# Optimization experiments

Measured on AMD Instinct MI355X. Metric: run time of the kernel, lower is better.

## Reference

```python
import jax, jax.numpy as jnp
import numpy as np

B, C, H, W = 4, 64, 64, 64  # in_dim hardcoded to 64 by the module's views


def _conv1x1(x, w, b):
    # x: [B,C,H,W], w: [O,C], b: [O]
    return jnp.einsum('bchw,oc->bohw', x, w) + b[None, :, None, None]


def _branch(x, wq, bq, wk, bk, wv, bv):
    b_, c_, h_, w_ = x.shape
    n = h_ * w_
    q = _conv1x1(x, wq, bq).reshape(b_, c_, n)
    k = _conv1x1(x, wk, bk).reshape(b_, c_, n)
    v = _conv1x1(x, wv, bv).reshape(b_, c_, n)
    # scores[b,i,j] = sum_c q[b,c,i] * k[b,c,j]  (no scale factor, as in source)
    s = jax.nn.softmax(jnp.einsum('bci,bcj->bij', q, k), axis=-1)  # [B,N,N]
    # out[b,c,j] = sum_i v[b,c,i] * s[b,i,j]
    return jnp.einsum('bci,bij->bcj', v, s).reshape(b_, c_, h_, w_)


def setup_inputs() -> dict:
    key = jax.random.key(0)
    ks = jax.random.split(key, 17)
    sc = 1.0 / np.sqrt(C)
    d = {'x': jax.random.normal(ks[0], (B, C, H, W), jnp.float32)}
    names = ['qh', 'kh', 'vh', 'ql', 'kl', 'vl']
    for i, nm in enumerate(names):
        d['W_' + nm] = jax.random.normal(ks[1 + 2 * i], (C, C), jnp.float32) * sc
        d['b_' + nm] = jax.random.normal(ks[2 + 2 * i], (C,), jnp.float32) * 0.01
    d['g1'] = jax.random.normal(ks[13], (1,), jnp.float32) * 0.5
    d['g2'] = jax.random.normal(ks[14], (1,), jnp.float32) * 0.5
    d['W_f'] = jax.random.normal(ks[15], (C, 2 * C), jnp.float32) * (1.0 / np.sqrt(2 * C))
    d['b_f'] = jax.random.normal(ks[16], (C,), jnp.float32) * 0.01
    return d


def reference(x, W_qh, b_qh, W_kh, b_kh, W_vh, b_vh, W_ql, b_ql, W_kl, b_kl, W_vl, b_vl, g1, g2, W_f, b_f):
    xh1 = g1[0] * _branch(x, W_qh, b_qh, W_kh, b_kh, W_vh, b_vh)
    xl1 = g2[0] * _branch(x, W_ql, b_ql, W_kl, b_kl, W_vl, b_vl)
    cat = jnp.concatenate([xh1, xl1], axis=1)  # [B,2C,H,W]
    return _conv1x1(cat, W_f, b_f)
```

## Files before the change

### kernel.cpp

```cpp
#include <hip/hip_runtime.h>

#define NN 4096
#define CD 64

typedef __attribute__((ext_vector_type(8))) short bf16x8;
typedef __attribute__((ext_vector_type(4))) float f32x4;

__device__ unsigned short g_Qh[2][4][NN][CD];
__device__ unsigned short g_Ql[2][4][NN][CD];
__device__ unsigned short g_Kh[2][4][NN][CD];
__device__ unsigned short g_Kl[2][4][NN][CD];
__device__ float          g_Vf[2][4][CD][NN];
__device__ unsigned short g_Vh[2][4][CD][NN];
__device__ unsigned short g_Vl[2][4][CD][NN];
__device__ float          g_O [2][4][CD][NN];
__device__ float          g_Z [2][4][NN];

__device__ inline f32x4 mfma16(bf16x8 a, bf16x8 b, f32x4 c) {
  return __builtin_amdgcn_mfma_f32_16x16x32_bf16(a, b, c, 0, 0, 0);
}

__device__ inline void split_bf(float x, unsigned short& h, unsigned short& l) {
  unsigned u = __builtin_bit_cast(unsigned, x);
  h = (unsigned short)(u >> 16);
  float hf = __builtin_bit_cast(float, u & 0xffff0000u);
  unsigned v = __builtin_bit_cast(unsigned, x - hf);
  v += 0x7fffu + ((v >> 16) & 1u);
  l = (unsigned short)(v >> 16);
}

__device__ inline void lds_barrier() {
  asm volatile("s_waitcnt lgkmcnt(0)\n\ts_barrier" ::: "memory");
}

struct ProjArgs {
  const float* x;
  const float* W[6];
  const float* bias[6];
};

__global__ __launch_bounds__(256) void proj_kernel(ProjArgs a) {
  __shared__ float Wt[64][68];
  __shared__ float bs[64];
  const int tid = threadIdx.x;
  const int m = blockIdx.z;
  const float* __restrict__ W = a.W[m];
#pragma unroll
  for (int k = 0; k < 16; ++k) {
    int t = k * 256 + tid;
    Wt[t & 63][t >> 6] = W[t];
  }
  if (tid < 64) bs[tid] = a.bias[m][tid];
  __syncthreads();

  const int b = blockIdx.y;
  const int n = (blockIdx.x << 6) + (tid & 63);
  const int og = tid >> 6;
  const float* __restrict__ xp = a.x + ((size_t)b * CD) * NN + n;

  float acc[16];
#pragma unroll
  for (int k = 0; k < 16; ++k) acc[k] = bs[og * 16 + k];

#pragma unroll 4
  for (int c = 0; c < 64; ++c) {
    float xv = xp[(size_t)c * NN];
    float w[16];
    *(float4*)&w[0]  = *(const float4*)&Wt[c][og * 16 + 0];
    *(float4*)&w[4]  = *(const float4*)&Wt[c][og * 16 + 4];
    *(float4*)&w[8]  = *(const float4*)&Wt[c][og * 16 + 8];
    *(float4*)&w[12] = *(const float4*)&Wt[c][og * 16 + 12];
#pragma unroll
    for (int k = 0; k < 16; ++k) acc[k] += w[k] * xv;
  }

  const int br = m / 3, kind = m % 3;
  if (kind == 2) {
    float* dst = &g_Vf[br][b][0][0] + n;
#pragma unroll
    for (int k = 0; k < 16; ++k) dst[(size_t)(og * 16 + k) * NN] = acc[k];
  } else {
    unsigned short hi[16], lo[16];
#pragma unroll
    for (int k = 0; k < 16; ++k) split_bf(acc[k], hi[k], lo[k]);
    unsigned short* dh = (kind == 0) ? &g_Qh[br][b][n][og * 16] : &g_Kh[br][b][n][og * 16];
    unsigned short* dl = (kind == 0) ? &g_Ql[br][b][n][og * 16] : &g_Kl[br][b][n][og * 16];
    *(uint4*)dh       = *(const uint4*)&hi[0];
    *(uint4*)(dh + 8) = *(const uint4*)&hi[8];
    *(uint4*)dl       = *(const uint4*)&lo[0];
    *(uint4*)(dl + 8) = *(const uint4*)&lo[8];
  }
}

__global__ __launch_bounds__(256) void pass1_kernel() {
  __shared__ unsigned short ks_h[2][64 * 64];
  __shared__ unsigned short ks_l[2][64 * 64];
  __shared__ float zbuf[2][64];

  const int tid = threadIdx.x;
  const int bid = blockIdx.x;
  const int img = bid & 7;
  const int br = img >> 2, b = img & 3;
  const int i0 = (bid >> 3) << 6;

  const int lane = tid & 63, w = tid >> 6;
  const int wi = w >> 1, wj = w & 1;
  const int lm = lane & 15, q = lane >> 4;

  const unsigned short* __restrict__ QhB = &g_Qh[br][b][0][0];
  const unsigned short* __restrict__ QlB = &g_Ql[br][b][0][0];
  const unsigned short* __restrict__ KhB = &g_Kh[br][b][0][0];
  const unsigned short* __restrict__ KlB = &g_Kl[br][b][0][0];

  bf16x8 qa[2][2][2];
#pragma unroll
  for (int it = 0; it < 2; ++it)
#pragma unroll
    for (int cs = 0; cs < 2; ++cs) {
      size_t off = (size_t)(i0 + wi * 32 + it * 16 + lm) * 64 + cs * 32 + q * 8;
      qa[it][cs][0] = *(const bf16x8*)(QhB + off);
      qa[it][cs][1] = *(const bf16x8*)(QlB + off);
    }

  const int r0 = tid >> 3, s0 = tid & 7;
  const int r1 = (256 + tid) >> 3, s1 = tid & 7;
  const int la0 = r0 * 128 + ((s0 * 16) ^ ((r0 & 7) << 4));
  const int la1 = r1 * 128 + ((s1 * 16) ^ ((r1 & 7) << 4));
  const size_t g0 = (size_t)r0 * 64 + s0 * 8;
  const size_t g1o = (size_t)r1 * 64 + s1 * 8;

  uint4 ph0, ph1, pl0, pl1;
  ph0 = *(const uint4*)(KhB + g0); ph1 = *(const uint4*)(KhB + g1o);
  pl0 = *(const uint4*)(KlB + g0); pl1 = *(const uint4*)(KlB + g1o);
  *(uint4*)((char*)ks_h[0] + la0) = ph0; *(uint4*)((char*)ks_h[0] + la1) = ph1;
  *(uint4*)((char*)ks_l[0] + la0) = pl0; *(uint4*)((char*)ks_l[0] + la1) = pl1;
  ph0 = *(const uint4*)(KhB + 4096 + g0); ph1 = *(const uint4*)(KhB + 4096 + g1o);
  pl0 = *(const uint4*)(KlB + 4096 + g0); pl1 = *(const uint4*)(KlB + 4096 + g1o);
  lds_barrier();

  float zacc[2][4];
#pragma unroll
  for (int it = 0; it < 2; ++it)
#pragma unroll
    for (int r = 0; r < 4; ++r) zacc[it][r] = 0.f;

  for (int t = 0; t < 64; ++t) {
    const int cur = t & 1;
    if (t < 63) {
      *(uint4*)((char*)ks_h[cur ^ 1] + la0) = ph0;
      *(uint4*)((char*)ks_h[cur ^ 1] + la1) = ph1;
      *(uint4*)((char*)ks_l[cur ^ 1] + la0) = pl0;
      *(uint4*)((char*)ks_l[cur ^ 1] + la1) = pl1;
      if (t < 62) {
        size_t tb = (size_t)(t + 2) * 4096;
        ph0 = *(const uint4*)(KhB + tb + g0); ph1 = *(const uint4*)(KhB + tb + g1o);
        pl0 = *(const uint4*)(KlB + tb + g0); pl1 = *(const uint4*)(KlB + tb + g1o);
      }
    }

    bf16x8 kb[2][2][2];
#pragma unroll
    for (int jt = 0; jt < 2; ++jt) {
      int row = wj * 32 + jt * 16 + lm;
      int rb = row * 128, sw = (row & 7) << 4;
#pragma unroll
      for (int cs = 0; cs < 2; ++cs) {
        int byte = rb + ((cs * 64 + q * 16) ^ sw);
        kb[jt][cs][0] = *(const bf16x8*)((const char*)ks_h[cur] + byte);
        kb[jt][cs][1] = *(const bf16x8*)((const char*)ks_l[cur] + byte);
      }
    }

    const f32x4 zf = {0.f, 0.f, 0.f, 0.f};
#pragma unroll
    for (int it = 0; it < 2; ++it)
#pragma unroll
      for (int jt = 0; jt < 2; ++jt) {
        f32x4 s = mfma16(qa[it][0][0], kb[jt][0][0], zf);
        s = mfma16(qa[it][1][0], kb[jt][1][0], s);
        s = mfma16(qa[it][0][0], kb[jt][0][1], s);
        s = mfma16(qa[it][1][0], kb[jt][1][1], s);
        s = mfma16(qa[it][0][1], kb[jt][0][0], s);
        s = mfma16(qa[it][1][1], kb[jt][1][0], s);
        zacc[it][0] += __expf(s[0]);
        zacc[it][1] += __expf(s[1]);
        zacc[it][2] += __expf(s[2]);
        zacc[it][3] += __expf(s[3]);
      }
    lds_barrier();
  }

#pragma unroll
  for (int mm = 1; mm < 16; mm <<= 1)
#pragma unroll
    for (int it = 0; it < 2; ++it)
#pragma unroll
      for (int r = 0; r < 4; ++r) zacc[it][r] += __shfl_xor(zacc[it][r], mm, 64);

  if (lm == 0) {
#pragma unroll
    for (int it = 0; it < 2; ++it)
#pragma unroll
      for (int r = 0; r < 4; ++r)
        zbuf[wj][wi * 32 + it * 16 + q * 4 + r] = zacc[it][r];
  }
  __syncthreads();
  if (tid < 64) g_Z[br][b][i0 + tid] = zbuf[0][tid] + zbuf[1][tid];
}

__global__ __launch_bounds__(256) void scalev_kernel(const float* __restrict__ g1,
                                                     const float* __restrict__ g2) {
  int idx = blockIdx.x * 256 + threadIdx.x;
  int i4 = idx & 1023;
  int c  = (idx >> 10) & 63;
  int b  = (idx >> 16) & 3;
  int br = idx >> 18;
  float g = br ? g2[0] : g1[0];
  const float4 z = *(const float4*)&g_Z[br][b][i4 * 4];
  float4 v = *(const float4*)&g_Vf[br][b][c][i4 * 4];
  float vv[4] = {v.x * g / z.x, v.y * g / z.y, v.z * g / z.z, v.w * g / z.w};
  unsigned short h[4], l[4];
#pragma unroll
  for (int r = 0; r < 4; ++r) split_bf(vv[r], h[r], l[r]);
  uint2 uh, ul;
  uh.x = (unsigned)h[0] | ((unsigned)h[1] << 16);
  uh.y = (unsigned)h[2] | ((unsigned)h[3] << 16);
  ul.x = (unsigned)l[0] | ((unsigned)l[1] << 16);
  ul.y = (unsigned)l[2] | ((unsigned)l[3] << 16);
  *(uint2*)&g_Vh[br][b][c][i4 * 4] = uh;
  *(uint2*)&g_Vl[br][b][c][i4 * 4] = ul;
}

__global__ __launch_bounds__(256, 2) void pass2_kernel() {
  __shared__ unsigned short pt_h[64 * 64];
  __shared__ unsigned short pt_l[64 * 64];

  const int tid = threadIdx.x;
  const int bid = blockIdx.x;
  const int img = bid & 7;
  const int br = img >> 2, b = img & 3;
  const int j0 = (bid >> 3) << 6;

  const int lane = tid & 63, w = tid >> 6;
  const int wi = w >> 1, wj = w & 1;
  const int lm = lane & 15, q = lane >> 4;

  const unsigned short* __restrict__ QhB = &g_Qh[br][b][0][0];
  const unsigned short* __restrict__ QlB = &g_Ql[br][b][0][0];
  const unsigned short* __restrict__ KhB = &g_Kh[br][b][0][0];
  const unsigned short* __restrict__ KlB = &g_Kl[br][b][0][0];
  const unsigned short* __restrict__ VhB = &g_Vh[br][b][0][0];
  const unsigned short* __restrict__ VlB = &g_Vl[br][b][0][0];

  bf16x8 kb[2][2][2];
#pragma unroll
  for (int jt = 0; jt < 2; ++jt)
#pragma unroll
    for (int cs = 0; cs < 2; ++cs) {
      size_t off = (size_t)(j0 + wj * 32 + jt * 16 + lm) * 64 + cs * 32 + q * 8;
      kb[jt][cs][0] = *(const bf16x8*)(KhB + off);
      kb[jt][cs][1] = *(const bf16x8*)(KlB + off);
    }

  bf16x8 qa[2][2][2];
  bf16x8 va[2][2][2];
  auto loadQ = [&](int ib) {
#pragma unroll
    for (int it = 0; it < 2; ++it)
#pragma unroll
      for (int cs = 0; cs < 2; ++cs) {
        size_t off = (size_t)(ib + wi * 32 + it * 16 + lm) * 64 + cs * 32 + q * 8;
        qa[it][cs][0] = *(const bf16x8*)(QhB + off);
        qa[it][cs][1] = *(const bf16x8*)(QlB + off);
      }
  };
  auto loadV = [&](int ib) {
#pragma unroll
    for (int ct = 0; ct < 2; ++ct)
#pragma unroll
      for (int ks = 0; ks < 2; ++ks) {
        size_t off = (size_t)(wi * 32 + ct * 16 + lm) * NN + ib + ks * 32 + q * 8;
        va[ct][ks][0] = *(const bf16x8*)(VhB + off);
        va[ct][ks][1] = *(const bf16x8*)(VlB + off);
      }
  };
  loadQ(0);
  loadV(0);

  f32x4 oacc[2][2];
#pragma unroll
  for (int ct = 0; ct < 2; ++ct)
#pragma unroll
    for (int jt = 0; jt < 2; ++jt) oacc[ct][jt] = (f32x4){0.f, 0.f, 0.f, 0.f};

  for (int t = 0; t < 64; ++t) {
    const int i0 = t << 6;
    const f32x4 zf = {0.f, 0.f, 0.f, 0.f};
    f32x4 sacc[2][2];
#pragma unroll
    for (int it = 0; it < 2; ++it)
#pragma unroll
      for (int jt = 0; jt < 2; ++jt) {
        f32x4 s = mfma16(qa[it][0][0], kb[jt][0][0], zf);
        s = mfma16(qa[it][1][0], kb[jt][1][0], s);
        s = mfma16(qa[it][0][0], kb[jt][0][1], s);
        s = mfma16(qa[it][1][0], kb[jt][1][1], s);
        s = mfma16(qa[it][0][1], kb[jt][0][0], s);
        s = mfma16(qa[it][1][1], kb[jt][1][0], s);
        sacc[it][jt] = s;
      }
    if (t < 63) loadQ(i0 + 64);

    uint2 wh[2][2], wl[2][2];
#pragma unroll
    for (int it = 0; it < 2; ++it)
#pragma unroll
      for (int jt = 0; jt < 2; ++jt) {
        unsigned short h[4], l[4];
#pragma unroll
        for (int r = 0; r < 4; ++r) {
          float e = __expf(sacc[it][jt][r]);
          split_bf(e, h[r], l[r]);
        }
        wh[it][jt].x = (unsigned)h[0] | ((unsigned)h[1] << 16);
        wh[it][jt].y = (unsigned)h[2] | ((unsigned)h[3] << 16);
        wl[it][jt].x = (unsigned)l[0] | ((unsigned)l[1] << 16);
        wl[it][jt].y = (unsigned)l[2] | ((unsigned)l[3] << 16);
      }

    lds_barrier();
#pragma unroll
    for (int it = 0; it < 2; ++it)
#pragma unroll
      for (int jt = 0; jt < 2; ++jt) {
        int row = wj * 32 + jt * 16 + lm;
        int byte = row * 128 + (((wi * 64) + it * 32 + q * 8) ^ ((row & 7) << 4));
        *(uint2*)((char*)pt_h + byte) = wh[it][jt];
        *(uint2*)((char*)pt_l + byte) = wl[it][jt];
      }
    lds_barrier();

    bf16x8 pb[2][2][2];
#pragma unroll
    for (int jt = 0; jt < 2; ++jt) {
      int row = wj * 32 + jt * 16 + lm;
      int rb = row * 128, sw = (row & 7) << 4;
#pragma unroll
      for (int ks = 0; ks < 2; ++ks) {
        int byte = rb + ((ks * 64 + q * 16) ^ sw);
        pb[jt][ks][0] = *(const bf16x8*)((const char*)pt_h + byte);
        pb[jt][ks][1] = *(const bf16x8*)((const char*)pt_l + byte);
      }
    }
#pragma unroll
    for (int ct = 0; ct < 2; ++ct)
#pragma unroll
      for (int jt = 0; jt < 2; ++jt) {
        f32x4 o = oacc[ct][jt];
        o = mfma16(va[ct][0][0], pb[jt][0][0], o);
        o = mfma16(va[ct][1][0], pb[jt][1][0], o);
        o = mfma16(va[ct][0][0], pb[jt][0][1], o);
        o = mfma16(va[ct][1][0], pb[jt][1][1], o);
        o = mfma16(va[ct][0][1], pb[jt][0][0], o);
        o = mfma16(va[ct][1][1], pb[jt][1][0], o);
        oacc[ct][jt] = o;
      }
    if (t < 63) loadV(i0 + 64);
  }

  float* __restrict__ Ob = &g_O[br][b][0][0];
#pragma unroll
  for (int ct = 0; ct < 2; ++ct)
#pragma unroll
    for (int jt = 0; jt < 2; ++jt)
#pragma unroll
      for (int r = 0; r < 4; ++r)
        Ob[(size_t)(wi * 32 + ct * 16 + q * 4 + r) * NN + j0 + wj * 32 + jt * 16 + lm] =
            oacc[ct][jt][r];
}

__global__ __launch_bounds__(256) void final_kernel(const float* __restrict__ Wf,
                                                    const float* __restrict__ bf,
                                                    float* __restrict__ out) {
  __shared__ float Wt[128][68];
  __shared__ float bs[64];
  const int tid = threadIdx.x;
#pragma unroll
  for (int k = 0; k < 32; ++k) {
    int t = k * 256 + tid;
    Wt[t & 127][t >> 7] = Wf[t];
  }
  if (tid < 64) bs[tid] = bf[tid];
  __syncthreads();

  const int b = blockIdx.y;
  const int n = (blockIdx.x << 6) + (tid & 63);
  const int og = tid >> 6;
  const float* __restrict__ Oh = &g_O[0][b][0][0];
  const float* __restrict__ Ol = &g_O[1][b][0][0];

  float acc[16];
#pragma unroll
  for (int k = 0; k < 16; ++k) acc[k] = bs[og * 16 + k];

#pragma unroll 4
  for (int c = 0; c < 64; ++c) {
    float xv = Oh[(size_t)c * NN + n];
    float w[16];
    *(float4*)&w[0]  = *(const float4*)&Wt[c][og * 16 + 0];
    *(float4*)&w[4]  = *(const float4*)&Wt[c][og * 16 + 4];
    *(float4*)&w[8]  = *(const float4*)&Wt[c][og * 16 + 8];
    *(float4*)&w[12] = *(const float4*)&Wt[c][og * 16 + 12];
#pragma unroll
    for (int k = 0; k < 16; ++k) acc[k] += w[k] * xv;
  }
#pragma unroll 4
  for (int c = 0; c < 64; ++c) {
    float xv = Ol[(size_t)c * NN + n];
    float w[16];
    *(float4*)&w[0]  = *(const float4*)&Wt[64 + c][og * 16 + 0];
    *(float4*)&w[4]  = *(const float4*)&Wt[64 + c][og * 16 + 4];
    *(float4*)&w[8]  = *(const float4*)&Wt[64 + c][og * 16 + 8];
    *(float4*)&w[12] = *(const float4*)&Wt[64 + c][og * 16 + 12];
#pragma unroll
    for (int k = 0; k < 16; ++k) acc[k] += w[k] * xv;
  }

  float* op = out + ((size_t)b * CD) * NN + n;
#pragma unroll
  for (int k = 0; k < 16; ++k) op[(size_t)(og * 16 + k) * NN] = acc[k];
}

extern "C" void kernel_launch(void* const* d_in, const int* in_sizes, int n_in,
                              void* d_out, int out_size, void* d_ws, size_t ws_size,
                              hipStream_t stream) {
  (void)in_sizes; (void)n_in; (void)d_ws; (void)ws_size; (void)out_size;

  ProjArgs pa;
  pa.x = (const float*)d_in[0];
  for (int m = 0; m < 6; ++m) {
    pa.W[m]    = (const float*)d_in[1 + 2 * m];
    pa.bias[m] = (const float*)d_in[2 + 2 * m];
  }
  const float* g1 = (const float*)d_in[13];
  const float* g2 = (const float*)d_in[14];
  const float* Wf = (const float*)d_in[15];
  const float* bf = (const float*)d_in[16];
  float* out = (float*)d_out;

  proj_kernel<<<dim3(64, 4, 6), 256, 0, stream>>>(pa);
  pass1_kernel<<<dim3(512), 256, 0, stream>>>();
  scalev_kernel<<<dim3(2048), 256, 0, stream>>>(g1, g2);
  pass2_kernel<<<dim3(512), 256, 0, stream>>>();
  final_kernel<<<dim3(64, 4), 256, 0, stream>>>(Wf, bf, out);
}
```

Measured before the change: 401.6 us.

## Split attention reduction dimension four ways across blocks with partial sums

After: 487.5 us. 21.4% more time.

```diff
diff --git a/kernel.cpp b/kernel.cpp
--- a/kernel.cpp
+++ b/kernel.cpp
@@ -13,8 +13,8 @@
 __device__ float          g_Vf[2][4][CD][NN];
 __device__ unsigned short g_Vh[2][4][CD][NN];
 __device__ unsigned short g_Vl[2][4][CD][NN];
-__device__ float          g_O [2][4][CD][NN];
-__device__ float          g_Z [2][4][NN];
+__device__ float          g_Op[4][2][4][CD][NN];
+__device__ float          g_Zp[4][2][4][NN];
 
 __device__ inline f32x4 mfma16(bf16x8 a, bf16x8 b, f32x4 c) {
   return __builtin_amdgcn_mfma_f32_16x16x32_bf16(a, b, c, 0, 0, 0);
@@ -93,15 +93,14 @@
 }
 
 __global__ __launch_bounds__(256) void pass1_kernel() {
-  __shared__ unsigned short ks_h[2][64 * 64];
-  __shared__ unsigned short ks_l[2][64 * 64];
   __shared__ float zbuf[2][64];
 
   const int tid = threadIdx.x;
   const int bid = blockIdx.x;
   const int img = bid & 7;
   const int br = img >> 2, b = img & 3;
-  const int i0 = (bid >> 3) << 6;
+  const int js = (bid >> 3) & 3;
+  const int i0 = (bid >> 5) << 6;
 
   const int lane = tid & 63, w = tid >> 6;
   const int wi = w >> 1, wj = w & 1;
@@ -122,52 +121,24 @@
       qa[it][cs][1] = *(const bf16x8*)(QlB + off);
     }
 
-  const int r0 = tid >> 3, s0 = tid & 7;
-  const int r1 = (256 + tid) >> 3, s1 = tid & 7;
-  const int la0 = r0 * 128 + ((s0 * 16) ^ ((r0 & 7) << 4));
-  const int la1 = r1 * 128 + ((s1 * 16) ^ ((r1 & 7) << 4));
-  const size_t g0 = (size_t)r0 * 64 + s0 * 8;
-  const size_t g1o = (size_t)r1 * 64 + s1 * 8;
-
-  uint4 ph0, ph1, pl0, pl1;
-  ph0 = *(const uint4*)(KhB + g0); ph1 = *(const uint4*)(KhB + g1o);
-  pl0 = *(const uint4*)(KlB + g0); pl1 = *(const uint4*)(KlB + g1o);
-  *(uint4*)((char*)ks_h[0] + la0) = ph0; *(uint4*)((char*)ks_h[0] + la1) = ph1;
-  *(uint4*)((char*)ks_l[0] + la0) = pl0; *(uint4*)((char*)ks_l[0] + la1) = pl1;
-  ph0 = *(const uint4*)(KhB + 4096 + g0); ph1 = *(const uint4*)(KhB + 4096 + g1o);
-  pl0 = *(const uint4*)(KlB + 4096 + g0); pl1 = *(const uint4*)(KlB + 4096 + g1o);
-  lds_barrier();
-
   float zacc[2][4];
 #pragma unroll
   for (int it = 0; it < 2; ++it)
 #pragma unroll
     for (int r = 0; r < 4; ++r) zacc[it][r] = 0.f;
 
-  for (int t = 0; t < 64; ++t) {
-    const int cur = t & 1;
-    if (t < 63) {
-      *(uint4*)((char*)ks_h[cur ^ 1] + la0) = ph0;
-      *(uint4*)((char*)ks_h[cur ^ 1] + la1) = ph1;
-      *(uint4*)((char*)ks_l[cur ^ 1] + la0) = pl0;
-      *(uint4*)((char*)ks_l[cur ^ 1] + la1) = pl1;
-      if (t < 62) {
-        size_t tb = (size_t)(t + 2) * 4096;
-        ph0 = *(const uint4*)(KhB + tb + g0); ph1 = *(const uint4*)(KhB + tb + g1o);
-        pl0 = *(const uint4*)(KlB + tb + g0); pl1 = *(const uint4*)(KlB + tb + g1o);
-      }
-    }
+  const int jwave = wj * 32 + lm;
+  for (int tt = 0; tt < 16; ++tt) {
+    const int jb = ((js << 4) + tt) << 6;
 
     bf16x8 kb[2][2][2];
 #pragma unroll
     for (int jt = 0; jt < 2; ++jt) {
-      int row = wj * 32 + jt * 16 + lm;
-      int rb = row * 128, sw = (row & 7) << 4;
+      size_t rowo = (size_t)(jb + jwave + jt * 16) * 64 + q * 8;
 #pragma unroll
       for (int cs = 0; cs < 2; ++cs) {
-        int byte = rb + ((cs * 64 + q * 16) ^ sw);
-        kb[jt][cs][0] = *(const bf16x8*)((const char*)ks_h[cur] + byte);
-        kb[jt][cs][1] = *(const bf16x8*)((const char*)ks_l[cur] + byte);
+        kb[jt][cs][0] = *(const bf16x8*)(KhB + rowo + cs * 32);
+        kb[jt][cs][1] = *(const bf16x8*)(KlB + rowo + cs * 32);
       }
     }
 
@@ -187,7 +158,6 @@
         zacc[it][2] += __expf(s[2]);
         zacc[it][3] += __expf(s[3]);
       }
-    lds_barrier();
   }
 
 #pragma unroll
@@ -205,7 +175,7 @@
         zbuf[wj][wi * 32 + it * 16 + q * 4 + r] = zacc[it][r];
   }
   __syncthreads();
-  if (tid < 64) g_Z[br][b][i0 + tid] = zbuf[0][tid] + zbuf[1][tid];
+  if (tid < 64) g_Zp[js][br][b][i0 + tid] = zbuf[0][tid] + zbuf[1][tid];
 }
 
 __global__ __launch_bounds__(256) void scalev_kernel(const float* __restrict__ g1,
@@ -216,7 +186,12 @@
   int b  = (idx >> 16) & 3;
   int br = idx >> 18;
   float g = br ? g2[0] : g1[0];
-  const float4 z = *(const float4*)&g_Z[br][b][i4 * 4];
+  float4 z0 = *(const float4*)&g_Zp[0][br][b][i4 * 4];
+  float4 z1 = *(const float4*)&g_Zp[1][br][b][i4 * 4];
+  float4 z2 = *(const float4*)&g_Zp[2][br][b][i4 * 4];
+  float4 z3 = *(const float4*)&g_Zp[3][br][b][i4 * 4];
+  float4 z = {z0.x + z1.x + z2.x + z3.x, z0.y + z1.y + z2.y + z3.y,
+              z0.z + z1.z + z2.z + z3.z, z0.w + z1.w + z2.w + z3.w};
   float4 v = *(const float4*)&g_Vf[br][b][c][i4 * 4];
   float vv[4] = {v.x * g / z.x, v.y * g / z.y, v.z * g / z.z, v.w * g / z.w};
   unsigned short h[4], l[4];
@@ -239,7 +214,8 @@
   const int bid = blockIdx.x;
   const int img = bid & 7;
   const int br = img >> 2, b = img & 3;
-  const int j0 = (bid >> 3) << 6;
+  const int is = (bid >> 3) & 3;
+  const int j0 = (bid >> 5) << 6;
 
   const int lane = tid & 63, w = tid >> 6;
   const int wi = w >> 1, wj = w & 1;
@@ -284,8 +260,9 @@
         va[ct][ks][1] = *(const bf16x8*)(VlB + off);
       }
   };
-  loadQ(0);
-  loadV(0);
+  const int ibase = is << 10;
+  loadQ(ibase);
+  loadV(ibase);
 
   f32x4 oacc[2][2];
 #pragma unroll
@@ -293,8 +270,8 @@
 #pragma unroll
     for (int jt = 0; jt < 2; ++jt) oacc[ct][jt] = (f32x4){0.f, 0.f, 0.f, 0.f};
 
-  for (int t = 0; t < 64; ++t) {
-    const int i0 = t << 6;
+  for (int tt = 0; tt < 16; ++tt) {
+    const int inext = ibase + ((tt + 1) << 6);
     const f32x4 zf = {0.f, 0.f, 0.f, 0.f};
     f32x4 sacc[2][2];
 #pragma unroll
@@ -309,7 +286,7 @@
         s = mfma16(qa[it][1][1], kb[jt][1][0], s);
         sacc[it][jt] = s;
       }
-    if (t < 63) loadQ(i0 + 64);
+    if (tt < 15) loadQ(inext);
 
     uint2 wh[2][2], wl[2][2];
 #pragma unroll
@@ -365,10 +342,10 @@
         o = mfma16(va[ct][1][1], pb[jt][1][0], o);
         oacc[ct][jt] = o;
       }
-    if (t < 63) loadV(i0 + 64);
-  }
-
-  float* __restrict__ Ob = &g_O[br][b][0][0];
+    if (tt < 15) loadV(inext);
+  }
+
+  float* __restrict__ Ob = &g_Op[is][br][b][0][0];
 #pragma unroll
   for (int ct = 0; ct < 2; ++ct)
 #pragma unroll
@@ -396,34 +373,27 @@
   const int b = blockIdx.y;
   const int n = (blockIdx.x << 6) + (tid & 63);
   const int og = tid >> 6;
-  const float* __restrict__ Oh = &g_O[0][b][0][0];
-  const float* __restrict__ Ol = &g_O[1][b][0][0];
+  const size_t PS = (size_t)2 * 4 * CD * NN;
 
   float acc[16];
 #pragma unroll
   for (int k = 0; k < 16; ++k) acc[k] = bs[og * 16 + k];
 
+#pragma unroll
+  for (int br = 0; br < 2; ++br) {
+    const float* __restrict__ Ob = &g_Op[0][br][b][0][0];
 #pragma unroll 4
-  for (int c = 0; c < 64; ++c) {
-    float xv = Oh[(size_t)c * NN + n];
-    float w[16];
-    *(float4*)&w[0]  = *(const float4*)&Wt[c][og * 16 + 0];
-    *(float4*)&w[4]  = *(const float4*)&Wt[c][og * 16 + 4];
-    *(float4*)&w[8]  = *(const float4*)&Wt[c][og * 16 + 8];
-    *(float4*)&w[12] = *(const float4*)&Wt[c][og * 16 + 12];
-#pragma unroll
-    for (int k = 0; k < 16; ++k) acc[k] += w[k] * xv;
-  }
-#pragma unroll 4
-  for (int c = 0; c < 64; ++c) {
-    float xv = Ol[(size_t)c * NN + n];
-    float w[16];
-    *(float4*)&w[0]  = *(const float4*)&Wt[64 + c][og * 16 + 0];
-    *(float4*)&w[4]  = *(const float4*)&Wt[64 + c][og * 16 + 4];
-    *(float4*)&w[8]  = *(const float4*)&Wt[64 + c][og * 16 + 8];
-    *(float4*)&w[12] = *(const float4*)&Wt[64 + c][og * 16 + 12];
-#pragma unroll
-    for (int k = 0; k < 16; ++k) acc[k] += w[k] * xv;
+    for (int c = 0; c < 64; ++c) {
+      const float* p = Ob + (size_t)c * NN + n;
+      float xv = p[0] + p[PS] + p[2 * PS] + p[3 * PS];
+      float wv[16];
+      *(float4*)&wv[0]  = *(const float4*)&Wt[br * 64 + c][og * 16 + 0];
+      *(float4*)&wv[4]  = *(const float4*)&Wt[br * 64 + c][og * 16 + 4];
+      *(float4*)&wv[8]  = *(const float4*)&Wt[br * 64 + c][og * 16 + 8];
+      *(float4*)&wv[12] = *(const float4*)&Wt[br * 64 + c][og * 16 + 12];
+#pragma unroll
+      for (int k = 0; k < 16; ++k) acc[k] += wv[k] * xv;
+    }
   }
 
   float* op = out + ((size_t)b * CD) * NN + n;
@@ -449,8 +419,8 @@
   float* out = (float*)d_out;
 
   proj_kernel<<<dim3(64, 4, 6), 256, 0, stream>>>(pa);
-  pass1_kernel<<<dim3(512), 256, 0, stream>>>();
+  pass1_kernel<<<dim3(2048), 256, 0, stream>>>();
   scalev_kernel<<<dim3(2048), 256, 0, stream>>>(g1, g2);
-  pass2_kernel<<<dim3(512), 256, 0, stream>>>();
+  pass2_kernel<<<dim3(2048), 256, 0, stream>>>();
   final_kernel<<<dim3(64, 4), 256, 0, stream>>>(Wf, bf, out);
 }
```
